# Performance work log

Measured on AMD Instinct MI355X. Metric: run time of the kernel, lower is better.

The kernel has to match this reference:

```python
import jax, jax.numpy as jnp
import numpy as np

TOTAL_LABELS = 21
TOTAL_POS = 128
TOTAL_NEG = 128
VARIANCES = jnp.asarray([0.1, 0.1, 0.2, 0.2], dtype=jnp.float32)


def _make_boxes(key, shape):
    # valid [y1,x1,y2,x2] boxes with y2>y1, x2>x1 in [0,1]
    k1, k2 = jax.random.split(key)
    lo = jax.random.uniform(k1, shape + (2,), dtype=jnp.float32) * 0.6
    sz = jax.random.uniform(k2, shape + (2,), dtype=jnp.float32) * 0.4 + 1e-3
    return jnp.concatenate([lo, lo + sz], axis=-1)


def setup_inputs() -> dict:
    key = jax.random.key(0)
    kr, kg, kl, kp, kn = jax.random.split(key, 5)
    B, N, M = 64, 3000, 128
    roi_bboxes = _make_boxes(kr, (B, N))
    gt_boxes = _make_boxes(kg, (B, M))
    gt_labels = jax.random.randint(kl, (B, M), 1, TOTAL_LABELS).astype(jnp.int32)
    maxval = max(TOTAL_POS, TOTAL_NEG) * 10  # matches tf.random.uniform(minval=1, maxval=10*count)
    rand_pos = jax.random.randint(kp, (B, N), 1, maxval).astype(jnp.int32)
    rand_neg = jax.random.randint(kn, (B, N), 1, maxval).astype(jnp.int32)
    return {"roi_bboxes": roi_bboxes, "gt_boxes": gt_boxes, "gt_labels": gt_labels,
            "rand_pos": rand_pos, "rand_neg": rand_neg}


def _iou_map(roi, gt):
    # roi: [B,N,4], gt: [B,M,4] -> iou: [B,N,M]
    r = roi[:, :, None, :]
    g = gt[:, None, :, :]
    iy1 = jnp.maximum(r[..., 0], g[..., 0])
    ix1 = jnp.maximum(r[..., 1], g[..., 1])
    iy2 = jnp.minimum(r[..., 2], g[..., 2])
    ix2 = jnp.minimum(r[..., 3], g[..., 3])
    inter = jnp.maximum(iy2 - iy1, 0.0) * jnp.maximum(ix2 - ix1, 0.0)
    area_r = (r[..., 2] - r[..., 0]) * (r[..., 3] - r[..., 1])
    area_g = (g[..., 2] - g[..., 0]) * (g[..., 3] - g[..., 1])
    return inter / (area_r + area_g - inter + 1e-7)


def _random_select(mask, rand_ints, count):
    # faithful port of train_utils.randomly_select_xyz_mask: rank by mask*rand, keep top `count`
    mult = mask.astype(jnp.int32) * rand_ints
    order = jnp.argsort(-mult, axis=-1)
    ranks = jnp.argsort(order, axis=-1)
    return mask & (ranks < count)


def _get_deltas(bboxes, gt):
    bw = bboxes[..., 3] - bboxes[..., 1]
    bh = bboxes[..., 2] - bboxes[..., 0]
    bcx = bboxes[..., 1] + 0.5 * bw
    bcy = bboxes[..., 0] + 0.5 * bh
    gw = gt[..., 3] - gt[..., 1]
    gh = gt[..., 2] - gt[..., 0]
    gcx = gt[..., 1] + 0.5 * gw
    gcy = gt[..., 0] + 0.5 * gh
    bw = jnp.where(bw == 0.0, 1e-3, bw)
    bh = jnp.where(bh == 0.0, 1e-3, bh)
    dx = jnp.where(gw == 0.0, 0.0, (gcx - bcx) / bw)
    dy = jnp.where(gh == 0.0, 0.0, (gcy - bcy) / bh)
    dw = jnp.where(gw == 0.0, 0.0, jnp.log(jnp.where(gw == 0.0, 1.0, gw / bw)))
    dh = jnp.where(gh == 0.0, 0.0, jnp.log(jnp.where(gh == 0.0, 1.0, gh / bh)))
    return jnp.stack([dy, dx, dh, dw], axis=-1)


def reference(roi_bboxes, gt_boxes, gt_labels, rand_pos, rand_neg):
    B, N = roi_bboxes.shape[:2]
    iou = _iou_map(roi_bboxes, gt_boxes)                      # [B,N,M]
    best_gt = jnp.argmax(iou, axis=2)                         # [B,N]
    best_iou = jnp.max(iou, axis=2)                           # [B,N]
    pos_mask = _random_select(best_iou > 0.5, rand_pos, TOTAL_POS)
    neg_mask = _random_select((best_iou < 0.5) & (best_iou > 0.1), rand_neg, TOTAL_NEG)
    gt_boxes_map = jnp.take_along_axis(gt_boxes, best_gt[:, :, None], axis=1)   # [B,N,4]
    expanded_gt_boxes = jnp.where(pos_mask[..., None], gt_boxes_map, 0.0)
    gt_labels_map = jnp.take_along_axis(gt_labels, best_gt, axis=1)             # [B,N]
    pos_gt_labels = jnp.where(pos_mask, gt_labels_map, -1)
    expanded_gt_labels = pos_gt_labels + neg_mask.astype(jnp.int32)
    deltas = _get_deltas(roi_bboxes, expanded_gt_boxes) / VARIANCES             # [B,N,4]
    roi_bbox_labels = jax.nn.one_hot(expanded_gt_labels, TOTAL_LABELS, dtype=deltas.dtype)  # [B,N,L]
    # broadcast-multiply scatter: place deltas into the slot of the assigned label
    roi_bbox_deltas = roi_bbox_labels[..., None] * deltas[:, :, None, :]        # [B,N,L,4]
    roi_bbox_deltas = roi_bbox_deltas.reshape(B, N * TOTAL_LABELS, 4)
    return (jax.lax.stop_gradient(roi_bbox_deltas), jax.lax.stop_gradient(roi_bbox_labels))
```

## Files before the change

kernel.cpp:

```cpp
#include <hip/hip_runtime.h>

#define BB 64
#define NN 3000
#define MM 128
#define NBINS 1280
#define NSEL 128

__global__ __launch_bounds__(256) void k1_iou(
    const float4* __restrict__ roi, const float4* __restrict__ gt,
    const int* __restrict__ gtl, const int* __restrict__ rpos,
    const int* __restrict__ rneg, int* __restrict__ packed,
    float4* __restrict__ deltas)
{
  #pragma clang fp contract(off)
  const int b = blockIdx.y;
  const int n = blockIdx.x * 256 + threadIdx.x;
  __shared__ float4 g[MM];
  __shared__ float  ga[MM];
  __shared__ int    gl[MM];
  if (threadIdx.x < MM) {
    float4 v = gt[b * MM + threadIdx.x];
    g[threadIdx.x]  = v;
    ga[threadIdx.x] = (v.z - v.x) * (v.w - v.y);
    gl[threadIdx.x] = gtl[b * MM + threadIdx.x];
  }
  __syncthreads();
  if (n >= NN) return;
  float4 r = roi[b * NN + n];
  float ar = (r.z - r.x) * (r.w - r.y);
  float best = -1.0f; int bi = 0;
  for (int m = 0; m < MM; ++m) {
    float4 gm = g[m];
    float iy1 = fmaxf(r.x, gm.x);
    float ix1 = fmaxf(r.y, gm.y);
    float iy2 = fminf(r.z, gm.z);
    float ix2 = fminf(r.w, gm.w);
    float inter = fmaxf(iy2 - iy1, 0.0f) * fmaxf(ix2 - ix1, 0.0f);
    float iou = inter / (ar + ga[m] - inter + 1e-7f);
    if (iou > best) { best = iou; bi = m; }
  }
  int pm = (best > 0.5f) ? rpos[b * NN + n] : 0;
  int nm = (best < 0.5f && best > 0.1f) ? rneg[b * NN + n] : 0;
  packed[b * NN + n] = pm | (nm << 11) | (gl[bi] << 22);

  float4 gg = g[bi];
  float bw = r.w - r.y, bh = r.z - r.x;
  float bcx = r.y + 0.5f * bw, bcy = r.x + 0.5f * bh;
  float gw = gg.w - gg.y, gh = gg.z - gg.x;
  float gcx = gg.y + 0.5f * gw, gcy = gg.x + 0.5f * gh;
  bw = (bw == 0.0f) ? 0.001f : bw;
  bh = (bh == 0.0f) ? 0.001f : bh;
  float dx = (gw == 0.0f) ? 0.0f : (gcx - bcx) / bw;
  float dy = (gh == 0.0f) ? 0.0f : (gcy - bcy) / bh;
  float dw = (gw == 0.0f) ? 0.0f : logf(gw / bw);
  float dh = (gh == 0.0f) ? 0.0f : logf(gh / bh);
  deltas[b * NN + n] = make_float4(dy / 0.1f, dx / 0.1f, dh / 0.2f, dw / 0.2f);
}

__global__ __launch_bounds__(1024) void k2_select(const int* __restrict__ packed,
                                                  int* __restrict__ labels)
{
  const int b = blockIdx.x;
  const int tid = threadIdx.x;
  __shared__ int sp[NN];
  __shared__ unsigned hist[2048];
  __shared__ unsigned csum[1024];
  __shared__ int sTvP, sQp, sTvN, sQn;

  for (int i = tid; i < NN; i += 1024) sp[i] = packed[b * NN + i];
  hist[tid] = 0; hist[tid + 1024] = 0;
  if (tid == 0) { sTvP = 0; sQp = 0; sTvN = 0; sQn = 0; }
  __syncthreads();
  for (int i = tid; i < NN; i += 1024) {
    int p = sp[i];
    int pm = p & 0x7FF, nm = (p >> 11) & 0x7FF;
    if (pm) atomicAdd(&hist[pm], 1u);
    if (nm) atomicAdd(&hist[nm], 0x10000u);
  }
  __syncthreads();
  for (int off = 1; off < 2048; off <<= 1) {
    unsigned a0 = hist[tid];
    unsigned a1 = hist[tid + 1024];
    if (tid + off < 2048)        a0 += hist[tid + off];
    if (tid + 1024 + off < 2048) a1 += hist[tid + 1024 + off];
    __syncthreads();
    hist[tid] = a0; hist[tid + 1024] = a1;
    __syncthreads();
  }
  for (int k = 0; k < 2; ++k) {
    int v = tid + k * 1024;
    if (v >= 1 && v < NBINS) {
      unsigned s0 = hist[v] & 0xFFFFu;
      unsigned s1 = hist[v + 1] & 0xFFFFu;
      if (s0 >= NSEL && s1 < NSEL) { sTvP = v; sQp = NSEL - (int)s1; }
      unsigned t0 = hist[v] >> 16;
      unsigned t1 = hist[v + 1] >> 16;
      if (t0 >= NSEL && t1 < NSEL) { sTvN = v; sQn = NSEL - (int)t1; }
    }
  }
  __syncthreads();
  const int Tp = sTvP, Tn = sTvN, Qp = sQp, Qn = sQn;
  const int n0 = tid * 3;
  unsigned cc = 0;
  for (int j = 0; j < 3; ++j) {
    int n = n0 + j;
    if (n < NN) {
      int p = sp[n];
      if (Tp && (p & 0x7FF) == Tp) cc += 1u;
      if (Tn && ((p >> 11) & 0x7FF) == Tn) cc += 0x10000u;
    }
  }
  csum[tid] = cc;
  __syncthreads();
  for (int off = 1; off < 1024; off <<= 1) {
    unsigned v = csum[tid];
    if (tid >= off) v += csum[tid - off];
    __syncthreads();
    csum[tid] = v;
    __syncthreads();
  }
  unsigned excl = csum[tid] - cc;
  int ep = (int)(excl & 0xFFFFu), en = (int)(excl >> 16);
  for (int j = 0; j < 3; ++j) {
    int n = n0 + j;
    if (n >= NN) break;
    int p = sp[n];
    int pm = p & 0x7FF, nm = (p >> 11) & 0x7FF;
    bool selp, seln;
    if (pm > Tp) selp = true;
    else if (pm == Tp && pm > 0) { selp = (ep < Qp); ep++; }
    else selp = false;
    if (nm > Tn) seln = true;
    else if (nm == Tn && nm > 0) { seln = (en < Qn); en++; }
    else seln = false;
    int lab = selp ? ((p >> 22) & 0x1F) : (seln ? 0 : -1);
    labels[b * NN + n] = lab;
  }
}

__global__ __launch_bounds__(256) void k3_expand(
    const int* __restrict__ labels, const float4* __restrict__ deltas,
    float4* __restrict__ out1, float* __restrict__ out2)
{
  const int total = BB * NN * 21;
  for (int u = blockIdx.x * blockDim.x + threadIdx.x; u < total;
       u += gridDim.x * blockDim.x) {
    int nl = u / 21;
    int c = u - nl * 21;
    int lab = labels[nl];
    float4 v = make_float4(0.f, 0.f, 0.f, 0.f);
    if (c == lab && lab > 0) v = deltas[nl];
    out1[u] = v;
    out2[u] = (c == lab) ? 1.0f : 0.0f;
  }
}

extern "C" void kernel_launch(void* const* d_in, const int* in_sizes, int n_in,
                              void* d_out, int out_size, void* d_ws, size_t ws_size,
                              hipStream_t stream) {
  const float4* roi = (const float4*)d_in[0];
  const float4* gt  = (const float4*)d_in[1];
  const int* gtl  = (const int*)d_in[2];
  const int* rpos = (const int*)d_in[3];
  const int* rneg = (const int*)d_in[4];

  char* ws = (char*)d_ws;
  int*    packed = (int*)ws;
  int*    labels = (int*)(ws + 768000);
  float4* deltas = (float4*)(ws + 1536000);

  float4* out1 = (float4*)d_out;
  float*  out2 = (float*)d_out + (size_t)BB * NN * 21 * 4;

  dim3 g1((NN + 255) / 256, BB);
  k1_iou<<<g1, 256, 0, stream>>>(roi, gt, gtl, rpos, rneg, packed, deltas);
  k2_select<<<BB, 1024, 0, stream>>>(packed, labels);
  k3_expand<<<4096, 256, 0, stream>>>(labels, deltas, out1, out2);
}
```

Measured before the change: 49.15 us.

## Fuse expand into select, zero deltas output in IoU kernel, wave-level scans

Removes the third kernel. The bulk zeroing of the large deltas output moves into the IoU kernel, where it runs alongside the compute-bound IoU loop. The select kernel now scatters only the selected deltas and writes the one-hot labels from shared memory. The block-wide Hillis-Steele scans over shared memory are replaced with per-lane serial prefix sums plus wavefront shuffles, which cuts many barriers. A trade-off is that the one-hot writes now come from only 64 blocks, which may limit bandwidth on that large output.

```diff
diff --git a/kernel.cpp b/kernel.cpp
--- a/kernel.cpp
+++ b/kernel.cpp
@@ -10,14 +10,17 @@
     const float4* __restrict__ roi, const float4* __restrict__ gt,
     const int* __restrict__ gtl, const int* __restrict__ rpos,
     const int* __restrict__ rneg, int* __restrict__ packed,
-    float4* __restrict__ deltas)
+    float4* __restrict__ deltas, float4* __restrict__ out1z)
 {
   #pragma clang fp contract(off)
   const int b = blockIdx.y;
   const int n = blockIdx.x * 256 + threadIdx.x;
+  const bool valid = (n < NN);
   __shared__ float4 g[MM];
   __shared__ float  ga[MM];
   __shared__ int    gl[MM];
+
+  float4 r = roi[b * NN + (valid ? n : 0)];
   if (threadIdx.x < MM) {
     float4 v = gt[b * MM + threadIdx.x];
     g[threadIdx.x]  = v;
@@ -25,10 +28,17 @@
     gl[threadIdx.x] = gtl[b * MM + threadIdx.x];
   }
   __syncthreads();
-  if (n >= NN) return;
-  float4 r = roi[b * NN + n];
+
+  {
+    const float4 z = make_float4(0.f, 0.f, 0.f, 0.f);
+    const int gid = (blockIdx.y * gridDim.x + blockIdx.x) * 256 + threadIdx.x;
+    for (int i = gid; i < BB * NN * 21; i += 768 * 256) out1z[i] = z;
+  }
+
+  if (!valid) return;
   float ar = (r.z - r.x) * (r.w - r.y);
   float best = -1.0f; int bi = 0;
+  #pragma unroll 4
   for (int m = 0; m < MM; ++m) {
     float4 gm = g[m];
     float iy1 = fmaxf(r.x, gm.x);
@@ -57,101 +67,117 @@
   deltas[b * NN + n] = make_float4(dy / 0.1f, dx / 0.1f, dh / 0.2f, dw / 0.2f);
 }
 
-__global__ __launch_bounds__(1024) void k2_select(const int* __restrict__ packed,
-                                                  int* __restrict__ labels)
+__global__ __launch_bounds__(1024) void k2_select(
+    const int* __restrict__ packed, const float4* __restrict__ deltas,
+    float4* __restrict__ out1, float* __restrict__ out2)
 {
   const int b = blockIdx.x;
   const int tid = threadIdx.x;
+  const int lane = tid & 63;
+  const int wave = tid >> 6;
   __shared__ int sp[NN];
-  __shared__ unsigned hist[2048];
-  __shared__ unsigned csum[1024];
-  __shared__ int sTvP, sQp, sTvN, sQn;
-
-  for (int i = tid; i < NN; i += 1024) sp[i] = packed[b * NN + i];
-  hist[tid] = 0; hist[tid + 1024] = 0;
-  if (tid == 0) { sTvP = 0; sQp = 0; sTvN = 0; sQn = 0; }
-  __syncthreads();
+  __shared__ unsigned hist[NBINS + 1];
+  __shared__ unsigned wsum[16];
+  __shared__ int sT[4];
+
+  for (int i = tid; i < NBINS + 1; i += 1024) hist[i] = 0;
+  if (tid == 0) { sT[0] = 0; sT[1] = 0; sT[2] = 0; sT[3] = 0; }
+  __syncthreads();
+
   for (int i = tid; i < NN; i += 1024) {
-    int p = sp[i];
+    int p = packed[b * NN + i];
+    sp[i] = p;
     int pm = p & 0x7FF, nm = (p >> 11) & 0x7FF;
     if (pm) atomicAdd(&hist[pm], 1u);
     if (nm) atomicAdd(&hist[nm], 0x10000u);
   }
   __syncthreads();
-  for (int off = 1; off < 2048; off <<= 1) {
-    unsigned a0 = hist[tid];
-    unsigned a1 = hist[tid + 1024];
-    if (tid + off < 2048)        a0 += hist[tid + off];
-    if (tid + 1024 + off < 2048) a1 += hist[tid + 1024 + off];
-    __syncthreads();
-    hist[tid] = a0; hist[tid + 1024] = a1;
-    __syncthreads();
-  }
-  for (int k = 0; k < 2; ++k) {
-    int v = tid + k * 1024;
-    if (v >= 1 && v < NBINS) {
-      unsigned s0 = hist[v] & 0xFFFFu;
-      unsigned s1 = hist[v + 1] & 0xFFFFu;
-      if (s0 >= NSEL && s1 < NSEL) { sTvP = v; sQp = NSEL - (int)s1; }
-      unsigned t0 = hist[v] >> 16;
-      unsigned t1 = hist[v + 1] >> 16;
-      if (t0 >= NSEL && t1 < NSEL) { sTvN = v; sQn = NSEL - (int)t1; }
-    }
-  }
-  __syncthreads();
-  const int Tp = sTvP, Tn = sTvN, Qp = sQp, Qn = sQn;
+
+  if (wave == 0) {
+    unsigned cs[21];
+    const int base = 1 + lane * 20;
+    cs[20] = 0;
+    #pragma unroll
+    for (int j = 19; j >= 0; --j) cs[j] = cs[j + 1] + hist[base + j];
+    unsigned tot = cs[0];
+    unsigned run = tot;
+    #pragma unroll
+    for (int off = 1; off < 64; off <<= 1) {
+      unsigned u = __shfl_down(run, off);
+      if (lane + off < 64) run += u;
+    }
+    unsigned above = run - tot;
+    #pragma unroll
+    for (int j = 0; j < 20; ++j) {
+      int bin = base + j;
+      unsigned s  = cs[j] + above;
+      unsigned sn = cs[j + 1] + above;
+      unsigned ps = s & 0xFFFFu, psn = sn & 0xFFFFu;
+      if (ps >= NSEL && psn < NSEL) { sT[0] = bin; sT[1] = NSEL - (int)psn; }
+      unsigned ns = s >> 16, nsn = sn >> 16;
+      if (ns >= NSEL && nsn < NSEL) { sT[2] = bin; sT[3] = NSEL - (int)nsn; }
+    }
+  }
+  __syncthreads();
+  const int Tp = sT[0], Qp = sT[1], Tn = sT[2], Qn = sT[3];
+
   const int n0 = tid * 3;
+  int p0 = 0, p1 = 0, p2 = 0;
+  if (n0     < NN) p0 = sp[n0];
+  if (n0 + 1 < NN) p1 = sp[n0 + 1];
+  if (n0 + 2 < NN) p2 = sp[n0 + 2];
   unsigned cc = 0;
-  for (int j = 0; j < 3; ++j) {
-    int n = n0 + j;
-    if (n < NN) {
-      int p = sp[n];
-      if (Tp && (p & 0x7FF) == Tp) cc += 1u;
-      if (Tn && ((p >> 11) & 0x7FF) == Tn) cc += 0x10000u;
-    }
-  }
-  csum[tid] = cc;
-  __syncthreads();
-  for (int off = 1; off < 1024; off <<= 1) {
-    unsigned v = csum[tid];
-    if (tid >= off) v += csum[tid - off];
-    __syncthreads();
-    csum[tid] = v;
-    __syncthreads();
-  }
-  unsigned excl = csum[tid] - cc;
+  {
+    int q[3] = {p0, p1, p2};
+    #pragma unroll
+    for (int j = 0; j < 3; ++j) {
+      int pm = q[j] & 0x7FF, nm = (q[j] >> 11) & 0x7FF;
+      if (Tp && pm == Tp) cc += 1u;
+      if (Tn && nm == Tn) cc += 0x10000u;
+    }
+  }
+  unsigned inc = cc;
+  #pragma unroll
+  for (int off = 1; off < 64; off <<= 1) {
+    unsigned u = __shfl_up(inc, off);
+    if (lane >= off) inc += u;
+  }
+  if (lane == 63) wsum[wave] = inc;
+  __syncthreads();
+  unsigned woff = 0;
+  for (int w = 0; w < wave; ++w) woff += wsum[w];
+  unsigned excl = woff + (inc - cc);
   int ep = (int)(excl & 0xFFFFu), en = (int)(excl >> 16);
+
+  int q[3] = {p0, p1, p2};
+  #pragma unroll
   for (int j = 0; j < 3; ++j) {
     int n = n0 + j;
     if (n >= NN) break;
-    int p = sp[n];
+    int p = q[j];
     int pm = p & 0x7FF, nm = (p >> 11) & 0x7FF;
-    bool selp, seln;
+    bool selp;
     if (pm > Tp) selp = true;
-    else if (pm == Tp && pm > 0) { selp = (ep < Qp); ep++; }
+    else if (pm && pm == Tp) { selp = (ep < Qp); ep++; }
     else selp = false;
+    bool seln;
     if (nm > Tn) seln = true;
-    else if (nm == Tn && nm > 0) { seln = (en < Qn); en++; }
+    else if (nm && nm == Tn) { seln = (en < Qn); en++; }
     else seln = false;
     int lab = selp ? ((p >> 22) & 0x1F) : (seln ? 0 : -1);
-    labels[b * NN + n] = lab;
-  }
-}
-
-__global__ __launch_bounds__(256) void k3_expand(
-    const int* __restrict__ labels, const float4* __restrict__ deltas,
-    float4* __restrict__ out1, float* __restrict__ out2)
-{
-  const int total = BB * NN * 21;
-  for (int u = blockIdx.x * blockDim.x + threadIdx.x; u < total;
-       u += gridDim.x * blockDim.x) {
-    int nl = u / 21;
-    int c = u - nl * 21;
-    int lab = labels[nl];
-    float4 v = make_float4(0.f, 0.f, 0.f, 0.f);
-    if (c == lab && lab > 0) v = deltas[nl];
-    out1[u] = v;
-    out2[u] = (c == lab) ? 1.0f : 0.0f;
+    sp[n] = lab;
+    if (lab > 0) {
+      size_t nl = (size_t)b * NN + n;
+      out1[nl * 21 + lab] = deltas[nl];
+    }
+  }
+  __syncthreads();
+
+  float* o2 = out2 + (size_t)b * NN * 21;
+  for (int u = tid; u < NN * 21; u += 1024) {
+    int n = u / 21;
+    int c = u - n * 21;
+    o2[u] = (c == sp[n]) ? 1.0f : 0.0f;
   }
 }
 
@@ -166,14 +192,12 @@
 
   char* ws = (char*)d_ws;
   int*    packed = (int*)ws;
-  int*    labels = (int*)(ws + 768000);
-  float4* deltas = (float4*)(ws + 1536000);
+  float4* deltas = (float4*)(ws + (1 << 20));
 
   float4* out1 = (float4*)d_out;
   float*  out2 = (float*)d_out + (size_t)BB * NN * 21 * 4;
 
   dim3 g1((NN + 255) / 256, BB);
-  k1_iou<<<g1, 256, 0, stream>>>(roi, gt, gtl, rpos, rneg, packed, deltas);
-  k2_select<<<BB, 1024, 0, stream>>>(packed, labels);
-  k3_expand<<<4096, 256, 0, stream>>>(labels, deltas, out1, out2);
+  k1_iou<<<g1, 256, 0, stream>>>(roi, gt, gtl, rpos, rneg, packed, deltas, out1);
+  k2_select<<<BB, 1024, 0, stream>>>(packed, deltas, out1, out2);
 }
```

New measurement: 48.08 us. -2.2%, faster.
